# Kernel tuning notes

Measured on AMD Instinct MI355X. Metric: run time of the kernel, lower is better.

## Reference

```python
import jax, jax.numpy as jnp
import numpy as np

B, S, D, H = 4, 2048, 1024, 16
HD = D // H

def setup_inputs() -> dict:
    key = jax.random.key(0)
    ks = jax.random.split(key, 11)
    s = 1.0 / np.sqrt(D)
    return {
        "query": jax.random.normal(ks[0], (B, S, D), jnp.float32),
        "key_": jax.random.normal(ks[1], (B, S, D), jnp.float32),
        "value": jax.random.normal(ks[2], (B, S, D), jnp.float32),
        "Wq": jax.random.normal(ks[3], (D, D), jnp.float32) * s,
        "bq": jax.random.normal(ks[4], (D,), jnp.float32) * s,
        "Wk": jax.random.normal(ks[5], (D, D), jnp.float32) * s,
        "bk": jax.random.normal(ks[6], (D,), jnp.float32) * s,
        "Wv": jax.random.normal(ks[7], (D, D), jnp.float32) * s,
        "bv": jax.random.normal(ks[8], (D,), jnp.float32) * s,
        "Wo": jax.random.normal(ks[9], (D, D), jnp.float32) * s,
        "bo": jax.random.normal(ks[10], (D,), jnp.float32) * s,
    }

def reference(query, key_, value, Wq, bq, Wk, bk, Wv, bv, Wo, bo):
    # projections (torch Linear: x @ W.T + b)
    q = query @ Wq.T + bq
    k = key_ @ Wk.T + bk
    v = value @ Wv.T + bv
    # [B,S,D] -> [B,H,S,hd]
    q = q.reshape(B, S, H, HD).transpose(0, 2, 1, 3)
    k = k.reshape(B, S, H, HD).transpose(0, 2, 1, 3)
    v = v.reshape(B, S, H, HD).transpose(0, 2, 1, 3)
    scale = HD ** 0.5
    scores = jnp.einsum('bhqd,bhkd->bhqk', q, k) / scale
    attn = jax.nn.softmax(scores, axis=-1)
    out = jnp.einsum('bhqk,bhkd->bhqd', attn, v)
    out = out.transpose(0, 2, 1, 3).reshape(B, S, D)
    return out @ Wo.T + bo
```

## Files before the change

kernel.cpp:

```cpp
#include <hip/hip_runtime.h>
#include <math.h>

#define B_ 4
#define S_ 2048
#define D_ 1024
#define H_ 16
#define HD_ 64
#define M_ (B_*S_)
#define BH_ (B_*H_)

typedef __attribute__((ext_vector_type(4))) float f32x4;
typedef _Float16 f16;
typedef __attribute__((ext_vector_type(8))) _Float16 f16x8;
typedef __attribute__((ext_vector_type(2))) __fp16 fp16x2_raw;
typedef unsigned short u16;

#define QSCALE 0.18033688011112042f

__device__ __forceinline__ unsigned pkh(float a, float b) {
    fp16x2_raw h = __builtin_amdgcn_cvt_pkrtz(a, b);
    unsigned r; __builtin_memcpy(&r, &h, 4);
    return r;
}
__device__ __forceinline__ uint2 f4_to_h4(float4 v) {
    uint2 r;
    r.x = pkh(v.x, v.y);
    r.y = pkh(v.z, v.w);
    return r;
}
__device__ __forceinline__ void gload_lds16(const void* g, void* l) {
    __builtin_amdgcn_global_load_lds(
        (const __attribute__((address_space(1))) void*)g,
        (__attribute__((address_space(3))) void*)l, 16, 0, 0);
}
#define EXP2(x) __builtin_amdgcn_exp2f(x)
#define MFMA16(a,b,c) __builtin_amdgcn_mfma_f32_16x16x32_f16((a),(b),(c),0,0,0)

__global__ __launch_bounds__(256) void conv_w_kernel(
    const float* __restrict__ w0, const float* __restrict__ w1,
    const float* __restrict__ w2, const float* __restrict__ w3,
    f16* __restrict__ out)
{
    const float* src = (blockIdx.y==0)?w0:(blockIdx.y==1)?w1:(blockIdx.y==2)?w2:w3;
    size_t off = (size_t)blockIdx.y << 20;
    size_t i = ((size_t)blockIdx.x*256 + threadIdx.x)*4;
    float4 v = *(const float4*)&src[i];
    *(uint2*)&out[off + i] = f4_to_h4(v);
}

__global__ __launch_bounds__(256) void conv_in_kernel(
    const float* __restrict__ src, f16* __restrict__ out)
{
    size_t i = ((size_t)blockIdx.x*256 + threadIdx.x)*4;
    float4 v = *(const float4*)&src[i];
    *(uint2*)&out[i] = f4_to_h4(v);
}

template<int MODE>
__global__ __launch_bounds__(256, 2) void gemm_mfma(
    const f16* __restrict__ Af16,
    const f16* __restrict__ Wh16,
    const float* __restrict__ bias,
    void* out0)
{
    __shared__ u16 Ah[128][32];
    __shared__ u16 Bh[128][32];

    const int t = threadIdx.x;
    const int lane = t & 63;
    const int w = t >> 6;
    const int wm = w >> 1, wn = w & 1;
    const int m0 = (int)(blockIdx.x >> 3) * 128;
    const int n0 = (int)(blockIdx.x & 7) * 128;

    const int srow_base = w*32;
    const int lrow_off  = lane >> 2;
    const int k8        = (lane & 3) * 8;

    f32x4 acc[4][4];
    #pragma unroll
    for (int i = 0; i < 4; ++i)
        #pragma unroll
        for (int j = 0; j < 4; ++j) { f32x4 z = {0.f,0.f,0.f,0.f}; acc[i][j] = z; }

    for (int k0 = 0; k0 < D_; k0 += 32) {
        __syncthreads();
        #pragma unroll
        for (int c = 0; c < 2; ++c) {
            int lrow = srow_base + c*16;
            int row = lrow + lrow_off;
            int kw = k8 ^ ((row & 3) << 3);
            size_t asrc;
            if constexpr (MODE == 3) {
                int m = m0 + row;
                int b = m >> 11, s = m & 2047;
                int kk = k0 + kw;
                asrc = (((size_t)b*H_ + (kk >> 6))*S_ + s)*HD_ + (kk & 63);
            } else {
                asrc = (size_t)(m0 + row)*D_ + k0 + kw;
            }
            gload_lds16(&Af16[asrc], &Ah[lrow][0]);
            gload_lds16(&Wh16[(size_t)(n0 + row)*D_ + k0 + kw], &Bh[lrow][0]);
        }
        __syncthreads();

        f16x8 ah[4], bh4[4];
        #pragma unroll
        for (int i = 0; i < 4; ++i) {
            int ml = wm*64 + i*16 + (lane & 15);
            int kwa = ((lane >> 4) * 8) ^ ((ml & 3) << 3);
            ah[i] = *(const f16x8*)&Ah[ml][kwa];
            int nl = wn*64 + i*16 + (lane & 15);
            int kwb = ((lane >> 4) * 8) ^ ((nl & 3) << 3);
            bh4[i] = *(const f16x8*)&Bh[nl][kwb];
        }
        __builtin_amdgcn_s_setprio(1);
        #pragma unroll
        for (int i = 0; i < 4; ++i)
            #pragma unroll
            for (int j = 0; j < 4; ++j)
                acc[i][j] = MFMA16(ah[i], bh4[j], acc[i][j]);
        __builtin_amdgcn_s_setprio(0);
    }

    #pragma unroll
    for (int i = 0; i < 4; ++i) {
        #pragma unroll
        for (int j = 0; j < 4; ++j) {
            int n = n0 + wn*64 + j*16 + (lane & 15);
            float bb = bias[n];
            int mbase = m0 + wm*64 + i*16 + (lane >> 4)*4;
            if constexpr (MODE == 3) {
                float* o = (float*)out0;
                #pragma unroll
                for (int r = 0; r < 4; ++r)
                    o[(size_t)(mbase + r)*D_ + n] = acc[i][j][r] + bb;
            } else if constexpr (MODE == 0) {
                f16* q = (f16*)out0;
                int b = mbase >> 11, h = n >> 6, hd = n & 63;
                size_t bh = (size_t)b*H_ + h;
                #pragma unroll
                for (int r = 0; r < 4; ++r) {
                    int s = (mbase + r) & 2047;
                    q[(bh*S_ + s)*64 + hd] = (f16)((acc[i][j][r] + bb) * QSCALE);
                }
            } else if constexpr (MODE == 1) {
                f16* oh = (f16*)out0;
                int b = mbase >> 11, h = n >> 6, hd = n & 63;
                size_t bh = (size_t)b*H_ + h;
                #pragma unroll
                for (int r = 0; r < 4; ++r) {
                    int s = (mbase + r) & 2047;
                    oh[(bh*S_ + s)*64 + hd] = (f16)(acc[i][j][r] + bb);
                }
            } else {
                int b = mbase >> 11, h = n >> 6, hd = n & 63;
                int s0 = mbase & 2047;
                uint2 ph;
                ph.x = pkh(acc[i][j][0] + bb, acc[i][j][1] + bb);
                ph.y = pkh(acc[i][j][2] + bb, acc[i][j][3] + bb);
                size_t idx = (((size_t)b*H_ + h)*HD_ + hd)*S_ + s0;
                *(uint2*)&((f16*)out0)[idx] = ph;
            }
        }
    }
}

__global__ __launch_bounds__(256, 2) void attn_mfma(
    const f16* __restrict__ kf,
    const f16* __restrict__ vtf,
    f16* qf)
{
    __shared__ u16 Kh[2][64][64];
    __shared__ u16 Vth[2][64][64];
    __shared__ u16 Ps[256][64];

    const int t = threadIdx.x;
    const int lane = t & 63;
    const int w = t >> 6;
    const int g = lane >> 4;
    const int l15 = lane & 15;

    const int lb = (int)blockIdx.x;
    const int logical = (lb & 7) * 64 + (lb >> 3);
    const int qtile = logical & 7;
    const int bh = logical >> 3;
    const size_t rowb = (size_t)bh * S_;
    const int q0 = qtile * 256;

    const int srow_off = lane >> 3;
    const int sd8      = (lane & 7) * 8;

    f16x8 qh[4][2];
    {
        int qr = q0 + w*64 + l15;
        #pragma unroll
        for (int mi = 0; mi < 4; ++mi)
            #pragma unroll
            for (int kk = 0; kk < 2; ++kk) {
                int d0 = kk*32 + g*8;
                qh[mi][kk] = *(const f16x8*)&qf[(rowb + qr + mi*16)*64 + d0];
            }
    }

    const f32x4 zero4 = {0.f, 0.f, 0.f, 0.f};
    f16x8 ones8;
    #pragma unroll
    for (int e = 0; e < 8; ++e) ones8[e] = (f16)1.0f;

    f32x4 O[4][4];
    f32x4 lacc[4];
    #pragma unroll
    for (int mi = 0; mi < 4; ++mi) {
        lacc[mi] = zero4;
        #pragma unroll
        for (int oj = 0; oj < 4; ++oj) O[mi][oj] = zero4;
    }

#define STAGE_KV(bsel, kt_) do { \
        _Pragma("unroll") \
        for (int c = 0; c < 2; ++c) { \
            int lrow = w*16 + c*8; \
            int row = lrow + srow_off; \
            int dsw = sd8 ^ ((row & 7) << 3); \
            size_t kg = (rowb + (kt_)*64 + row)*64 + dsw; \
            size_t vg = ((size_t)bh*HD_ + row)*S_ + (kt_)*64 + dsw; \
            gload_lds16(&kf[kg],  &Kh[bsel][lrow][0]); \
            gload_lds16(&vtf[vg], &Vth[bsel][lrow][0]); \
        } \
    } while (0)

    STAGE_KV(0, 0);

    const int NT = S_/64;
    for (int kt = 0; kt < NT; ++kt) {
        const int cur = kt & 1;
        if (kt + 1 < NT) {
            STAGE_KV(cur ^ 1, kt + 1);
            asm volatile("s_waitcnt vmcnt(4)" ::: "memory");
        } else {
            asm volatile("s_waitcnt vmcnt(0)" ::: "memory");
        }
        __builtin_amdgcn_s_barrier();

        f32x4 sa[4][4];
        {
            f16x8 kb[4];
            #pragma unroll
            for (int k4 = 0; k4 < 4; ++k4) {
                int kv = k4*16 + l15;
                int dw = (g*8) ^ ((kv & 7) << 3);
                kb[k4] = *(const f16x8*)&Kh[cur][kv][dw];
            }
            __builtin_amdgcn_s_setprio(1);
            #pragma unroll
            for (int k4 = 0; k4 < 4; ++k4)
                #pragma unroll
                for (int qt = 0; qt < 4; ++qt)
                    sa[k4][qt] = MFMA16(kb[k4], qh[qt][0], zero4);
            __builtin_amdgcn_s_setprio(0);
        }
        {
            f16x8 kb[4];
            #pragma unroll
            for (int k4 = 0; k4 < 4; ++k4) {
                int kv = k4*16 + l15;
                int dw = (32 + g*8) ^ ((kv & 7) << 3);
                kb[k4] = *(const f16x8*)&Kh[cur][kv][dw];
            }
            __builtin_amdgcn_s_setprio(1);
            #pragma unroll
            for (int k4 = 0; k4 < 4; ++k4)
                #pragma unroll
                for (int qt = 0; qt < 4; ++qt)
                    sa[k4][qt] = MFMA16(kb[k4], qh[qt][1], sa[k4][qt]);
            __builtin_amdgcn_s_setprio(0);
        }

        u16* Pflat = &Ps[0][0];
        #pragma unroll
        for (int qt = 0; qt < 4; ++qt) {
            int qw = w*64 + qt*16 + l15;
            int prow = qw * 64;
            int sw = (qw & 7) << 3;
            #pragma unroll
            for (int k4 = 0; k4 < 4; ++k4) {
                float p0 = EXP2(sa[k4][qt][0]);
                float p1 = EXP2(sa[k4][qt][1]);
                float p2 = EXP2(sa[k4][qt][2]);
                float p3 = EXP2(sa[k4][qt][3]);
                uint2 pk;
                pk.x = pkh(p0, p1);
                pk.y = pkh(p2, p3);
                int kvb = k4*16 + g*4;
                *(uint2*)&Pflat[prow + (kvb ^ sw)] = pk;
            }
        }

        #pragma unroll
        for (int k2 = 0; k2 < 2; ++k2) {
            f16x8 pa[4], vb[4];
            #pragma unroll
            for (int mi = 0; mi < 4; ++mi) {
                int q = w*64 + mi*16 + l15;
                int kw = (k2*32 + g*8) ^ ((q & 7) << 3);
                pa[mi] = *(const f16x8*)&Pflat[q*64 + kw];
            }
            #pragma unroll
            for (int oj = 0; oj < 4; ++oj) {
                int hd = oj*16 + l15;
                int kw = (k2*32 + g*8) ^ ((hd & 7) << 3);
                vb[oj] = *(const f16x8*)&Vth[cur][hd][kw];
            }
            __builtin_amdgcn_s_setprio(1);
            #pragma unroll
            for (int mi = 0; mi < 4; ++mi) {
                #pragma unroll
                for (int oj = 0; oj < 4; ++oj)
                    O[mi][oj] = MFMA16(pa[mi], vb[oj], O[mi][oj]);
                lacc[mi] = MFMA16(pa[mi], ones8, lacc[mi]);
            }
            __builtin_amdgcn_s_setprio(0);
        }

        __builtin_amdgcn_s_barrier();
    }
#undef STAGE_KV

    #pragma unroll
    for (int mi = 0; mi < 4; ++mi)
        #pragma unroll
        for (int r = 0; r < 4; ++r) {
            float iv = 1.f / lacc[mi][r];
            int q = q0 + w*64 + mi*16 + g*4 + r;
            #pragma unroll
            for (int oj = 0; oj < 4; ++oj) {
                int hd = oj*16 + l15;
                qf[(rowb + q)*HD_ + hd] = (f16)(O[mi][oj][r] * iv);
            }
        }
}

extern "C" void kernel_launch(void* const* d_in, const int* in_sizes, int n_in,
                              void* d_out, int out_size, void* d_ws, size_t ws_size,
                              hipStream_t stream) {
    const float* query = (const float*)d_in[0];
    const float* key_  = (const float*)d_in[1];
    const float* value = (const float*)d_in[2];
    const float* Wq    = (const float*)d_in[3];
    const float* bq    = (const float*)d_in[4];
    const float* Wk    = (const float*)d_in[5];
    const float* bk    = (const float*)d_in[6];
    const float* Wv    = (const float*)d_in[7];
    const float* bv    = (const float*)d_in[8];
    const float* Wo    = (const float*)d_in[9];
    const float* bo    = (const float*)d_in[10];
    float* out = (float*)d_out;

    char* wsb = (char*)d_ws;
    const size_t SZ_H = (size_t)BH_*S_*64*2;
    f16* qf   = (f16*)wsb;
    f16* kf   = (f16*)(wsb + SZ_H);
    f16* vtf  = (f16*)(wsb + 2*SZ_H);
    f16* in16 = (f16*)(wsb + 3*SZ_H);
    f16* W16  = (f16*)(wsb + 4*SZ_H);

    dim3 gGemm(512);
    dim3 gAttn(512);
    dim3 gConv(8192);

    conv_w_kernel<<<dim3(1024,4), 256, 0, stream>>>(Wq, Wk, Wv, Wo, W16);
    conv_in_kernel<<<gConv, 256, 0, stream>>>(query, in16);
    gemm_mfma<0><<<gGemm, 256, 0, stream>>>(in16, W16 + ((size_t)0<<20), bq, qf);
    conv_in_kernel<<<gConv, 256, 0, stream>>>(key_, in16);
    gemm_mfma<1><<<gGemm, 256, 0, stream>>>(in16, W16 + ((size_t)1<<20), bk, kf);
    conv_in_kernel<<<gConv, 256, 0, stream>>>(value, in16);
    gemm_mfma<2><<<gGemm, 256, 0, stream>>>(in16, W16 + ((size_t)2<<20), bv, vtf);
    attn_mfma<<<gAttn, 256, 0, stream>>>(kf, vtf, qf);
    gemm_mfma<3><<<gGemm, 256, 0, stream>>>(qf, W16 + ((size_t)3<<20), bo, out);
}
```

Measured before the change: 227.0 us.

## Double-buffer GEMM LDS tiles and batch input conversions into one launch

The projection GEMM now prefetches the next K-slice into a second LDS buffer while computing on the current one, using explicit vmcnt waits and barriers instead of load-then-sync. The three fp32-to-fp16 input conversions are merged into a single launch writing separate buffers, with the key and value copies placed in the output buffer as scratch. This hides global load latency and removes launch gaps, at the cost of doubled LDS use, which may affect occupancy.

```diff
diff --git a/kernel.cpp b/kernel.cpp
--- a/kernel.cpp
+++ b/kernel.cpp
@@ -48,9 +48,13 @@
     *(uint2*)&out[off + i] = f4_to_h4(v);
 }
 
-__global__ __launch_bounds__(256) void conv_in_kernel(
-    const float* __restrict__ src, f16* __restrict__ out)
+__global__ __launch_bounds__(256) void conv_in3_kernel(
+    const float* __restrict__ s0, const float* __restrict__ s1,
+    const float* __restrict__ s2,
+    f16* __restrict__ o0, f16* __restrict__ o1, f16* __restrict__ o2)
 {
+    const float* src = (blockIdx.y==0)?s0:(blockIdx.y==1)?s1:s2;
+    f16* out = (blockIdx.y==0)?o0:(blockIdx.y==1)?o1:o2;
     size_t i = ((size_t)blockIdx.x*256 + threadIdx.x)*4;
     float4 v = *(const float4*)&src[i];
     *(uint2*)&out[i] = f4_to_h4(v);
@@ -63,8 +67,8 @@
     const float* __restrict__ bias,
     void* out0)
 {
-    __shared__ u16 Ah[128][32];
-    __shared__ u16 Bh[128][32];
+    __shared__ u16 Ah[2][128][32];
+    __shared__ u16 Bh[2][128][32];
 
     const int t = threadIdx.x;
     const int lane = t & 63;
@@ -83,36 +87,48 @@
         #pragma unroll
         for (int j = 0; j < 4; ++j) { f32x4 z = {0.f,0.f,0.f,0.f}; acc[i][j] = z; }
 
-    for (int k0 = 0; k0 < D_; k0 += 32) {
-        __syncthreads();
-        #pragma unroll
-        for (int c = 0; c < 2; ++c) {
-            int lrow = srow_base + c*16;
-            int row = lrow + lrow_off;
-            int kw = k8 ^ ((row & 3) << 3);
-            size_t asrc;
-            if constexpr (MODE == 3) {
-                int m = m0 + row;
-                int b = m >> 11, s = m & 2047;
-                int kk = k0 + kw;
-                asrc = (((size_t)b*H_ + (kk >> 6))*S_ + s)*HD_ + (kk & 63);
-            } else {
-                asrc = (size_t)(m0 + row)*D_ + k0 + kw;
-            }
-            gload_lds16(&Af16[asrc], &Ah[lrow][0]);
-            gload_lds16(&Wh16[(size_t)(n0 + row)*D_ + k0 + kw], &Bh[lrow][0]);
-        }
-        __syncthreads();
+#define G_STAGE(bsel, k0_) do { \
+        _Pragma("unroll") \
+        for (int c = 0; c < 2; ++c) { \
+            int lrow = srow_base + c*16; \
+            int row = lrow + lrow_off; \
+            int kw = k8 ^ ((row & 3) << 3); \
+            size_t asrc; \
+            if constexpr (MODE == 3) { \
+                int m = m0 + row; \
+                int b = m >> 11, s = m & 2047; \
+                int kk = (k0_) + kw; \
+                asrc = (((size_t)b*H_ + (kk >> 6))*S_ + s)*HD_ + (kk & 63); \
+            } else { \
+                asrc = (size_t)(m0 + row)*D_ + (k0_) + kw; \
+            } \
+            gload_lds16(&Af16[asrc], &Ah[bsel][lrow][0]); \
+            gload_lds16(&Wh16[(size_t)(n0 + row)*D_ + (k0_) + kw], &Bh[bsel][lrow][0]); \
+        } \
+    } while (0)
+
+    G_STAGE(0, 0);
+
+    const int NK = D_/32;
+    for (int step = 0; step < NK; ++step) {
+        const int cur = step & 1;
+        if (step + 1 < NK) {
+            G_STAGE(cur ^ 1, (step + 1) * 32);
+            asm volatile("s_waitcnt vmcnt(4)" ::: "memory");
+        } else {
+            asm volatile("s_waitcnt vmcnt(0)" ::: "memory");
+        }
+        __builtin_amdgcn_s_barrier();
 
         f16x8 ah[4], bh4[4];
         #pragma unroll
         for (int i = 0; i < 4; ++i) {
             int ml = wm*64 + i*16 + (lane & 15);
             int kwa = ((lane >> 4) * 8) ^ ((ml & 3) << 3);
-            ah[i] = *(const f16x8*)&Ah[ml][kwa];
+            ah[i] = *(const f16x8*)&Ah[cur][ml][kwa];
             int nl = wn*64 + i*16 + (lane & 15);
             int kwb = ((lane >> 4) * 8) ^ ((nl & 3) << 3);
-            bh4[i] = *(const f16x8*)&Bh[nl][kwb];
+            bh4[i] = *(const f16x8*)&Bh[cur][nl][kwb];
         }
         __builtin_amdgcn_s_setprio(1);
         #pragma unroll
@@ -121,7 +137,10 @@
             for (int j = 0; j < 4; ++j)
                 acc[i][j] = MFMA16(ah[i], bh4[j], acc[i][j]);
         __builtin_amdgcn_s_setprio(0);
-    }
+
+        __builtin_amdgcn_s_barrier();
+    }
+#undef G_STAGE
 
     #pragma unroll
     for (int i = 0; i < 4; ++i) {
@@ -362,20 +381,19 @@
     f16* qf   = (f16*)wsb;
     f16* kf   = (f16*)(wsb + SZ_H);
     f16* vtf  = (f16*)(wsb + 2*SZ_H);
-    f16* in16 = (f16*)(wsb + 3*SZ_H);
+    f16* in_q = (f16*)(wsb + 3*SZ_H);
     f16* W16  = (f16*)(wsb + 4*SZ_H);
+    f16* in_k = (f16*)d_out;
+    f16* in_v = in_k + (size_t)M_*D_;
 
     dim3 gGemm(512);
     dim3 gAttn(512);
-    dim3 gConv(8192);
 
     conv_w_kernel<<<dim3(1024,4), 256, 0, stream>>>(Wq, Wk, Wv, Wo, W16);
-    conv_in_kernel<<<gConv, 256, 0, stream>>>(query, in16);
-    gemm_mfma<0><<<gGemm, 256, 0, stream>>>(in16, W16 + ((size_t)0<<20), bq, qf);
-    conv_in_kernel<<<gConv, 256, 0, stream>>>(key_, in16);
-    gemm_mfma<1><<<gGemm, 256, 0, stream>>>(in16, W16 + ((size_t)1<<20), bk, kf);
-    conv_in_kernel<<<gConv, 256, 0, stream>>>(value, in16);
-    gemm_mfma<2><<<gGemm, 256, 0, stream>>>(in16, W16 + ((size_t)2<<20), bv, vtf);
+    conv_in3_kernel<<<dim3(8192,3), 256, 0, stream>>>(query, key_, value, in_q, in_k, in_v);
+    gemm_mfma<0><<<gGemm, 256, 0, stream>>>(in_q, W16 + ((size_t)0<<20), bq, qf);
+    gemm_mfma<1><<<gGemm, 256, 0, stream>>>(in_k, W16 + ((size_t)1<<20), bk, kf);
+    gemm_mfma<2><<<gGemm, 256, 0, stream>>>(in_v, W16 + ((size_t)2<<20), bv, vtf);
     attn_mfma<<<gAttn, 256, 0, stream>>>(kf, vtf, qf);
     gemm_mfma<3><<<gGemm, 256, 0, stream>>>(qf, W16 + ((size_t)3<<20), bo, out);
 }
```

Result: no change. 226.6 us (-0.2%).
